# Performance work log

Hardware: AMD Instinct MI355X
Metric: run time of the kernel (lower is better)

Reference implementation:

```python
import jax, jax.numpy as jnp
import numpy as np

E = 8        # num_experts
H = 2048     # hidden_size
I = 1408     # expert_intermediate_size
SI = 2816    # shared intermediate = I * num_shared_experts
K = 2        # top_k


def swiglu(x):
    a, b = jnp.split(x, 2, axis=-1)
    return jax.nn.silu(a) * b


def setup_inputs() -> dict:
    key = jax.random.key(0)
    ks = jax.random.split(key, 8)
    hidden_states = jax.random.normal(ks[0], (2, 2048, H), dtype=jnp.float32)
    topk_weight = jax.random.uniform(ks[1], (2, 2048, K), dtype=jnp.float32)
    topk_idx = jax.random.randint(ks[2], (2, 2048, K), 0, E)
    s = 0.02
    W1 = jax.random.normal(ks[3], (E, H, 2 * I), dtype=jnp.float32) * s   # per-expert h->2i (swiglu)
    W2 = jax.random.normal(ks[4], (E, I, H), dtype=jnp.float32) * s      # per-expert i->h
    Ws1 = jax.random.normal(ks[5], (H, 2 * SI), dtype=jnp.float32) * s   # shared h->2*si
    Ws2 = jax.random.normal(ks[6], (SI, H), dtype=jnp.float32) * s       # shared si->h
    return {"hidden_states": hidden_states, "topk_weight": topk_weight,
            "W1": W1, "W2": W2, "Ws1": Ws1, "Ws2": Ws2, "topk_idx": topk_idx}


def reference(hidden_states, topk_weight, W1, W2, Ws1, Ws2, topk_idx):
    orig_shape = hidden_states.shape
    x = hidden_states.reshape(-1, H)                       # [T, h]
    T = x.shape[0]
    # run every expert on every token (dense, faithful to masked-loop math)
    h1 = jnp.einsum('th,ehf->tef', x, W1)                  # [T, E, 2i]
    act = swiglu(h1)                                       # [T, E, i]
    expert_out = jnp.einsum('tei,eih->teh', act, W2)       # [T, E, h]
    # combine weights: comb[t,e] = sum_j topk_weight[t,j] * 1[topk_idx[t,j]==e]
    onehot = jax.nn.one_hot(topk_idx.reshape(T, K), E, dtype=x.dtype)  # [T, K, E]
    comb = jnp.einsum('tk,tke->te', topk_weight.reshape(T, K), onehot)
    y = jnp.einsum('te,teh->th', comb, expert_out)         # [T, h]
    # shared experts MLP on identity
    y = y + swiglu(x @ Ws1) @ Ws2
    return y.reshape(orig_shape)
```

## Files before the change

### kernel.cpp

```cpp
#include <hip/hip_runtime.h>
#include <cmath>

#define E_    8
#define H_    2048
#define IH    1408
#define I2    2816
#define SIH   2816
#define SI2   5632
#define KTOP  2
#define T_    4096
#define NA    (T_*KTOP)
#define MAXR  (NA + E_*256)

typedef __attribute__((ext_vector_type(4)))  short  short4v;
typedef __attribute__((ext_vector_type(8)))  __bf16 bf16x8;
typedef __attribute__((ext_vector_type(4)))  float  f32x4;
typedef unsigned short bf16r;

__device__ __forceinline__ bf16r f2b(float f) {
    unsigned int u = __float_as_uint(f);
    return (bf16r)((u + 0x7FFFu + ((u >> 16) & 1u)) >> 16);
}
__device__ __forceinline__ float b2f(bf16r s) {
    return __uint_as_float(((unsigned int)s) << 16);
}

__device__ __forceinline__ void gld16(const bf16r* g, void* l) {
    __builtin_amdgcn_global_load_lds((const __attribute__((address_space(1))) void*)g,
                                     (__attribute__((address_space(3))) void*)l, 16, 0, 0);
}
__device__ __forceinline__ void barrier_raw() { asm volatile("s_barrier" ::: "memory"); }
template<int N> __device__ __forceinline__ void vmwait() {
    asm volatile("s_waitcnt vmcnt(%0)" :: "i"(N) : "memory");
}

__global__ void route_k(const int* __restrict__ idx, const float* __restrict__ tw,
                        int* __restrict__ route) {
    __shared__ int cnt[E_], cur[E_], offs[E_ + 1];
    int t = threadIdx.x;
    if (t < E_) { cnt[t] = 0; cur[t] = 0; }
    float* wrow = (float*)(route + 64 + MAXR);
    for (int i = t; i < MAXR; i += 256) { route[64 + i] = -1; wrow[i] = 0.f; }
    __syncthreads();
    for (int a = t; a < NA; a += 256) atomicAdd(&cnt[idx[a]], 1);
    __syncthreads();
    if (t == 0) {
        int run = 0;
        for (int e = 0; e < E_; e++) { offs[e] = run; run += ((cnt[e] + 255) >> 8) << 8; }
        offs[E_] = run;
    }
    __syncthreads();
    for (int a = t; a < NA; a += 256) {
        int e = idx[a];
        int p = atomicAdd(&cur[e], 1);
        int r = offs[e] + p;
        route[64 + r] = a / KTOP;
        wrow[r] = tw[a];
    }
    if (t <= E_) route[32 + t] = offs[t];
}

__global__ void cvt_k(const float* __restrict__ in, bf16r* __restrict__ out, int n4) {
    int i = blockIdx.x * 256 + threadIdx.x;
    if (i < n4) {
        float4 v = ((const float4*)in)[i];
        short4v o;
        o[0] = (short)f2b(v.x); o[1] = (short)f2b(v.y);
        o[2] = (short)f2b(v.z); o[3] = (short)f2b(v.w);
        ((short4v*)out)[i] = o;
    }
}

__global__ void tconv_k(const float* __restrict__ in, bf16r* __restrict__ out,
                        int R, int C, long ims, long oms) {
    __shared__ bf16r tile[64][65];
    const float* inp = in + blockIdx.z * ims;
    bf16r* outp = out + blockIdx.z * oms;
    int c0 = blockIdx.x * 64, r0 = blockIdx.y * 64;
    int tx = threadIdx.x, ty = threadIdx.y;
    #pragma unroll
    for (int j = 0; j < 16; j++) {
        int r = ty * 16 + j;
        tile[r][tx] = f2b(inp[(long)(r0 + r) * C + c0 + tx]);
    }
    __syncthreads();
    #pragma unroll
    for (int j = 0; j < 16; j++) {
        int c = ty * 16 + j;
        outp[(long)(c0 + c) * R + r0 + tx] = tile[tx][c];
    }
}


#define PH_READ_A(MH) { _Pragma("unroll") for (int i4 = 0; i4 < 4; i4++) \
                        _Pragma("unroll") for (int kk = 0; kk < 2; kk++) \
                            af[i4][kk] = rdA(cur, (MH), i4, kk); }
#define PH_READ_B(NH) { _Pragma("unroll") for (int j2 = 0; j2 < NJ2; j2++) \
                        _Pragma("unroll") for (int kk = 0; kk < 2; kk++) \
                            bf[(NH)][j2][kk] = rdB(cur, (NH), j2, kk); }
#define PH_MMA(MH, NH) { __builtin_amdgcn_s_setprio(1); \
    _Pragma("unroll") for (int i4 = 0; i4 < 4; i4++) \
    _Pragma("unroll") for (int j2 = 0; j2 < NJ2; j2++) \
    _Pragma("unroll") for (int kk = 0; kk < 2; kk++) \
        acc[(MH)][(NH)][i4][j2] = __builtin_amdgcn_mfma_f32_16x16x32_bf16( \
            af[i4][kk], bf[(NH)][j2][kk], acc[(MH)][(NH)][i4][j2], 0, 0, 0); \
    __builtin_amdgcn_s_setprio(0); }

template<int BNv, int KD, bool GATHER, bool ROUTED, bool PAIRED, int EPI>
__global__ __launch_bounds__(512, 2)
void g8_k(const bf16r* __restrict__ A,
          const bf16r* __restrict__ Bt, long bstride, int F,
          void* __restrict__ Cv, int ldc,
          const int* __restrict__ off, const int* __restrict__ perm,
          const float* __restrict__ wrow, int gM)
{
    constexpr int NJ2 = BNv / 128;
    constexpr int LB  = NJ2;
    constexpr int BHE = BNv * 32;
    constexpr int NT  = KD / 64;
    constexpr int W0  = (BNv == 256) ? 10 : 8;
    constexpr int W2  = (BNv == 256) ? 12 : 9;
    static_assert(!PAIRED || NJ2 == 2, "paired swiglu needs BN=256");
    static_assert(NT >= 3 && (NT & 1) == 0, "even K-tile count");

    extern __shared__ __align__(16) char smem[];
    bf16r* lA = (bf16r*)smem;
    bf16r* lB = (bf16r*)(smem + 65536);

    int nwg = gridDim.x, orig = blockIdx.x;
    int q8 = nwg >> 3, r8 = nwg & 7, xc = orig & 7, o8 = orig >> 3;
    int wgid = (xc < r8 ? xc * (q8 + 1) : r8 * (q8 + 1) + (xc - r8) * q8) + o8;
    int mt = wgid % gM, nt = wgid / gM;
    const int r0 = mt * 256;
    int e = 0;
    if (ROUTED) {
        if (r0 >= off[E_]) return;
        while (e + 1 < E_ && off[e + 1] <= r0) e++;
    }
    const bf16r* Bte = ROUTED ? Bt + (long)e * bstride : Bt;

    const int tid  = threadIdx.x;
    const int lane = tid & 63;
    const int wave = tid >> 6;
    const int wm = wave >> 2, wn = wave & 3;
    const int ml = lane & 15, kg = lane >> 4;
    const int srw  = lane >> 3;
    const int ksrc = ((lane & 7) ^ srw) * 8;

    const bf16r* pA[2][2];
    #pragma unroll
    for (int h = 0; h < 2; h++)
        #pragma unroll
        for (int l = 0; l < 2; l++) {
            int gr = r0 + h * 128 + (wave + 8 * l) * 8 + srw;
            long rw = gr;
            if (GATHER) { int tk = perm[gr]; rw = (tk < 0) ? 0 : tk; }
            pA[h][l] = A + rw * (long)KD + ksrc;
        }
    const bf16r* pB[2][LB];
    #pragma unroll
    for (int nh = 0; nh < 2; nh++)
        #pragma unroll
        for (int l = 0; l < LB; l++) {
            int lr = (wave + 8 * l) * 8 + srw;
            long gr;
            if (PAIRED) {
                int wn_ = lr >> 5, j2_ = (lr >> 4) & 1, ml_ = lr & 15;
                gr = (long)(nt * 128 + nh * 64 + wn_ * 16 + ml_) + (j2_ ? (long)F : 0L);
            } else if (NJ2 == 2) gr = (long)(nt * 256 + nh * 128 + lr);
            else                 gr = (long)(nt * 128 + nh * 64  + lr);
            pB[nh][l] = Bte + gr * (long)KD + ksrc;
        }

    auto stgA = [&](int b, int h, int kp) {
        char* d = smem + ((b * 2 + h) << 14) + (wave << 10);
        gld16(pA[h][0] + kp, d);
        gld16(pA[h][1] + kp, d + 8192);
    };
    auto stgB = [&](int b, int nh, int kp) {
        char* d = smem + 65536 + (b * 2 + nh) * (BHE * 2) + (wave << 10);
        gld16(pB[nh][0] + kp, d);
        if constexpr (LB == 2) gld16(pB[nh][1] + kp, d + 8192);
    };
    auto rdA = [&](int b, int mh, int i4, int kk) -> bf16x8 {
        int row = wm * 64 + i4 * 16 + ml;
        int u = kk * 4 + kg;
        int ee = ((b * 2 + mh) << 13) + row * 64 + ((u ^ (row & 7)) << 3);
        return *(const bf16x8*)&lA[ee];
    };
    auto rdB = [&](int b, int nh, int j2, int kk) -> bf16x8 {
        int rb = (NJ2 == 2) ? (wn * 32 + j2 * 16 + ml) : (wn * 16 + ml);
        int u = kk * 4 + kg;
        int ee = (b * 2 + nh) * BHE + rb * 64 + ((u ^ (rb & 7)) << 3);
        return *(const bf16x8*)&lB[ee];
    };

    f32x4 acc[2][2][4][NJ2];
    #pragma unroll
    for (int a0 = 0; a0 < 2; a0++)
        #pragma unroll
        for (int b0 = 0; b0 < 2; b0++)
            #pragma unroll
            for (int i = 0; i < 4; i++)
                #pragma unroll
                for (int j = 0; j < NJ2; j++)
                    acc[a0][b0][i][j] = f32x4{0.f, 0.f, 0.f, 0.f};

    bf16x8 af[4][2], bf[2][NJ2][2];

    vmwait<0>();
    stgA(0, 0, 0); stgB(0, 0, 0); stgB(0, 1, 0);
    stgA(0, 1, 0);
    stgA(1, 0, 64); stgB(1, 0, 64); stgB(1, 1, 64);

    #pragma unroll 2
    for (int t = 0; t < NT; t++) {
        const int cur = t & 1, nxt = cur ^ 1;
        const int k1 = ((t + 1 < NT) ? (t + 1) : (NT - 1)) * 64;
        const int k2 = ((t + 2 < NT) ? (t + 2) : (NT - 1)) * 64;
        stgA(nxt, 1, k1);
        vmwait<W0>(); barrier_raw();
        PH_READ_A(0); PH_READ_B(0);
        PH_MMA(0, 0);
        barrier_raw();
        stgA(cur, 0, k2);
        barrier_raw();
        PH_READ_B(1);
        PH_MMA(0, 1);
        barrier_raw();
        stgB(cur, 0, k2);
        vmwait<W2>(); barrier_raw();
        PH_READ_A(1);
        PH_MMA(1, 0);
        barrier_raw();
        stgB(cur, 1, k2);
        barrier_raw();
        PH_MMA(1, 1);
        barrier_raw();
    }

    const long colbase = (long)nt * (PAIRED ? 128 : BNv);
    #pragma unroll
    for (int mh = 0; mh < 2; mh++)
        #pragma unroll
        for (int i4 = 0; i4 < 4; i4++)
            #pragma unroll
            for (int rr = 0; rr < 4; rr++) {
                long row = (long)r0 + mh * 128 + wm * 64 + i4 * 16 + kg * 4 + rr;
                if constexpr (PAIRED) {
                    bf16r* ap = (bf16r*)Cv + row * (long)ldc + colbase;
                    #pragma unroll
                    for (int nh = 0; nh < 2; nh++) {
                        float g = acc[mh][nh][i4][0][rr];
                        float u = acc[mh][nh][i4][1][rr];
                        float s = g / (1.0f + __expf(-g));
                        ap[nh * 64 + wn * 16 + ml] = f2b(s * u);
                    }
                } else if constexpr (EPI == 1) {
                    float* cp = (float*)Cv + row * (long)ldc + colbase;
                    #pragma unroll
                    for (int nh = 0; nh < 2; nh++)
                        #pragma unroll
                        for (int j2 = 0; j2 < NJ2; j2++)
                            cp[nh * (BNv / 2) + wn * (BNv / 8) + j2 * 16 + ml] =
                                acc[mh][nh][i4][j2][rr];
                } else {
                    int tok = perm[row];
                    if (tok >= 0) {
                        float w = wrow[row];
                        float* cp = (float*)Cv + (long)tok * ldc + colbase;
                        #pragma unroll
                        for (int nh = 0; nh < 2; nh++)
                            #pragma unroll
                            for (int j2 = 0; j2 < NJ2; j2++)
                                atomicAdd(&cp[nh * (BNv / 2) + wn * (BNv / 8) + j2 * 16 + ml],
                                          w * acc[mh][nh][i4][j2][rr]);
                    }
                }
            }
}

#undef PH_READ_A
#undef PH_READ_B
#undef PH_MMA

extern "C" void kernel_launch(void* const* d_in, const int* in_sizes, int n_in,
                              void* d_out, int out_size, void* d_ws, size_t ws_size,
                              hipStream_t stream)
{
    const float* x   = (const float*)d_in[0];
    const float* tw  = (const float*)d_in[1];
    const float* W1  = (const float*)d_in[2];
    const float* W2  = (const float*)d_in[3];
    const float* Ws1 = (const float*)d_in[4];
    const float* Ws2 = (const float*)d_in[5];
    const int*   tix = (const int*)d_in[6];
    float* out = (float*)d_out;

    char* ws    = (char*)d_ws;
    int*  route = (int*)ws;
    const int*   off  = route + 32;
    const int*   perm = route + 64;
    const float* wrow = (const float*)(route + 64 + MAXR);

    bf16r* xb   = (bf16r*)(ws + (1u << 20));
    bf16r* W1t  = xb   + (size_t)T_ * H_;
    bf16r* W2t  = W1t  + (size_t)E_ * I2 * H_;
    bf16r* Ws1t = W2t  + (size_t)E_ * H_ * IH;
    bf16r* Ws2t = Ws1t + (size_t)SI2 * H_;
    bf16r* actS = Ws2t + (size_t)H_ * SIH;
    bf16r* actR = actS + (size_t)T_ * SIH;

    static bool attr_done = false;
    if (!attr_done) {
        hipFuncSetAttribute(reinterpret_cast<const void*>(&g8_k<256,2048,false,false,true,0>),
                            hipFuncAttributeMaxDynamicSharedMemorySize, 131072);
        hipFuncSetAttribute(reinterpret_cast<const void*>(&g8_k<256,2048,true,true,true,0>),
                            hipFuncAttributeMaxDynamicSharedMemorySize, 131072);
        hipFuncSetAttribute(reinterpret_cast<const void*>(&g8_k<128,2816,false,false,false,1>),
                            hipFuncAttributeMaxDynamicSharedMemorySize, 98304);
        hipFuncSetAttribute(reinterpret_cast<const void*>(&g8_k<256,1408,false,true,false,2>),
                            hipFuncAttributeMaxDynamicSharedMemorySize, 131072);
        attr_done = true;
    }

    route_k<<<1, 256, 0, stream>>>(tix, tw, route);

    cvt_k<<<(T_ * H_ / 4 + 255) / 256, 256, 0, stream>>>(x, xb, T_ * H_ / 4);
    tconv_k<<<dim3(SI2 / 64, H_ / 64, 1), dim3(64, 4), 0, stream>>>(Ws1, Ws1t, H_, SI2, 0, 0);
    tconv_k<<<dim3(H_ / 64, SIH / 64, 1), dim3(64, 4), 0, stream>>>(Ws2, Ws2t, SIH, H_, 0, 0);
    tconv_k<<<dim3(I2 / 64, H_ / 64, E_), dim3(64, 4), 0, stream>>>(W1, W1t, H_, I2,
                                                                    (long)H_ * I2, (long)I2 * H_);
    tconv_k<<<dim3(H_ / 64, IH / 64, E_), dim3(64, 4), 0, stream>>>(W2, W2t, IH, H_,
                                                                    (long)IH * H_, (long)H_ * IH);

    g8_k<256,2048,false,false,true,0><<<dim3((SIH/128)*(T_/256)), dim3(512), 131072, stream>>>(
        xb, Ws1t, 0, SIH, actS, SIH, nullptr, nullptr, nullptr, T_/256);
    g8_k<128,2816,false,false,false,1><<<dim3((H_/128)*(T_/256)), dim3(512), 98304, stream>>>(
        actS, Ws2t, 0, 0, out, H_, nullptr, nullptr, nullptr, T_/256);
    g8_k<256,2048,true,true,true,0><<<dim3((IH/128)*(MAXR/256)), dim3(512), 131072, stream>>>(
        xb, W1t, (long)I2 * H_, IH, actR, IH, off, perm, nullptr, MAXR/256);
    g8_k<256,1408,false,true,false,2><<<dim3((H_/256)*(MAXR/256)), dim3(512), 131072, stream>>>(
        actR, W2t, (long)H_ * IH, 0, out, H_, off, perm, wrow, MAXR/256);
}
```

Baseline: 813.1 us.

## Restructure GEMM pipeline prefetch ordering and replace scatter atomics with bf16 staging plus combine

The GEMM main loop is reordered so LDS fragment reads for each phase are issued before the next global-to-LDS stage, with double-buffered A fragments and a uniform vmcnt wait, aiming to overlap LDS reads with MFMA and memory traffic better. The routed down-projection epilogue no longer does fp32 atomicAdd scatters into the output. It writes weighted results in bf16 to a per-row staging buffer that reuses the W1t region, and a new comb_k kernel gathers the two rows per token and adds them to the output. This removes atomic contention but adds an extra kernel plus bf16 rounding of the expert outputs before the sum.

```diff
diff --git a/kernel.cpp b/kernel.cpp
--- a/kernel.cpp
+++ b/kernel.cpp
@@ -40,6 +40,7 @@
     int t = threadIdx.x;
     if (t < E_) { cnt[t] = 0; cur[t] = 0; }
     float* wrow = (float*)(route + 64 + MAXR);
+    int* pos = route + 64 + 2 * MAXR;
     for (int i = t; i < MAXR; i += 256) { route[64 + i] = -1; wrow[i] = 0.f; }
     __syncthreads();
     for (int a = t; a < NA; a += 256) atomicAdd(&cnt[idx[a]], 1);
@@ -56,6 +57,7 @@
         int r = offs[e] + p;
         route[64 + r] = a / KTOP;
         wrow[r] = tw[a];
+        pos[a] = r;
     }
     if (t <= E_) route[32 + t] = offs[t];
 }
@@ -91,19 +93,35 @@
     }
 }
 
+__global__ void comb_k(float* __restrict__ out, const bf16r* __restrict__ outR,
+                       const int* __restrict__ pos) {
+    int i = blockIdx.x * 256 + threadIdx.x;
+    int t  = i >> 9;
+    int c4 = i & 511;
+    int p0 = pos[2 * t], p1 = pos[2 * t + 1];
+    float4 o = ((float4*)out)[i];
+    short4v r0 = ((const short4v*)(outR + (long)p0 * H_))[c4];
+    short4v r1 = ((const short4v*)(outR + (long)p1 * H_))[c4];
+    o.x += b2f((bf16r)r0[0]) + b2f((bf16r)r1[0]);
+    o.y += b2f((bf16r)r0[1]) + b2f((bf16r)r1[1]);
+    o.z += b2f((bf16r)r0[2]) + b2f((bf16r)r1[2]);
+    o.w += b2f((bf16r)r0[3]) + b2f((bf16r)r1[3]);
+    ((float4*)out)[i] = o;
+}
+
 
 #define PH_READ_A(MH) { _Pragma("unroll") for (int i4 = 0; i4 < 4; i4++) \
                         _Pragma("unroll") for (int kk = 0; kk < 2; kk++) \
-                            af[i4][kk] = rdA(cur, (MH), i4, kk); }
+                            af[(MH)][i4][kk] = rdA(cur, (MH), i4, kk); }
 #define PH_READ_B(NH) { _Pragma("unroll") for (int j2 = 0; j2 < NJ2; j2++) \
                         _Pragma("unroll") for (int kk = 0; kk < 2; kk++) \
-                            bf[(NH)][j2][kk] = rdB(cur, (NH), j2, kk); }
+                            bfr[(NH)][j2][kk] = rdB(cur, (NH), j2, kk); }
 #define PH_MMA(MH, NH) { __builtin_amdgcn_s_setprio(1); \
     _Pragma("unroll") for (int i4 = 0; i4 < 4; i4++) \
     _Pragma("unroll") for (int j2 = 0; j2 < NJ2; j2++) \
     _Pragma("unroll") for (int kk = 0; kk < 2; kk++) \
         acc[(MH)][(NH)][i4][j2] = __builtin_amdgcn_mfma_f32_16x16x32_bf16( \
-            af[i4][kk], bf[(NH)][j2][kk], acc[(MH)][(NH)][i4][j2], 0, 0, 0); \
+            af[(MH)][i4][kk], bfr[(NH)][j2][kk], acc[(MH)][(NH)][i4][j2], 0, 0, 0); \
     __builtin_amdgcn_s_setprio(0); }
 
 template<int BNv, int KD, bool GATHER, bool ROUTED, bool PAIRED, int EPI>
@@ -118,10 +136,9 @@
     constexpr int LB  = NJ2;
     constexpr int BHE = BNv * 32;
     constexpr int NT  = KD / 64;
-    constexpr int W0  = (BNv == 256) ? 10 : 8;
-    constexpr int W2  = (BNv == 256) ? 12 : 9;
+    constexpr int VW  = 4 + 2 * LB;
     static_assert(!PAIRED || NJ2 == 2, "paired swiglu needs BN=256");
-    static_assert(NT >= 3 && (NT & 1) == 0, "even K-tile count");
+    static_assert(NT >= 4 && (NT & 1) == 0, "even K-tile count >= 4");
 
     extern __shared__ __align__(16) char smem[];
     bf16r* lA = (bf16r*)smem;
@@ -206,38 +223,42 @@
                 for (int j = 0; j < NJ2; j++)
                     acc[a0][b0][i][j] = f32x4{0.f, 0.f, 0.f, 0.f};
 
-    bf16x8 af[4][2], bf[2][NJ2][2];
+    bf16x8 af[2][4][2], bfr[2][NJ2][2];
 
     vmwait<0>();
-    stgA(0, 0, 0); stgB(0, 0, 0); stgB(0, 1, 0);
-    stgA(0, 1, 0);
-    stgA(1, 0, 64); stgB(1, 0, 64); stgB(1, 1, 64);
+    stgA(0, 0, 0); stgB(0, 0, 0); stgB(0, 1, 0); stgA(0, 1, 0);
+    stgA(1, 0, 64); stgB(1, 0, 64);
+    vmwait<LB + 2>(); barrier_raw();
 
     #pragma unroll 2
     for (int t = 0; t < NT; t++) {
         const int cur = t & 1, nxt = cur ^ 1;
         const int k1 = ((t + 1 < NT) ? (t + 1) : (NT - 1)) * 64;
         const int k2 = ((t + 2 < NT) ? (t + 2) : (NT - 1)) * 64;
+        PH_READ_A(0); PH_READ_B(0);
+        stgB(nxt, 1, k1);
+        vmwait<VW>();
+        barrier_raw();
+        PH_MMA(0, 0);
+        barrier_raw();
+        PH_READ_B(1);
         stgA(nxt, 1, k1);
-        vmwait<W0>(); barrier_raw();
-        PH_READ_A(0); PH_READ_B(0);
-        PH_MMA(0, 0);
-        barrier_raw();
+        vmwait<VW>();
+        barrier_raw();
+        PH_MMA(0, 1);
+        barrier_raw();
+        PH_READ_A(1);
         stgA(cur, 0, k2);
         barrier_raw();
-        PH_READ_B(1);
-        PH_MMA(0, 1);
+        PH_MMA(1, 0);
         barrier_raw();
         stgB(cur, 0, k2);
-        vmwait<W2>(); barrier_raw();
-        PH_READ_A(1);
-        PH_MMA(1, 0);
-        barrier_raw();
-        stgB(cur, 1, k2);
+        vmwait<VW>();
         barrier_raw();
         PH_MMA(1, 1);
         barrier_raw();
     }
+    vmwait<0>();
 
     const long colbase = (long)nt * (PAIRED ? 128 : BNv);
     #pragma unroll
@@ -268,13 +289,13 @@
                     int tok = perm[row];
                     if (tok >= 0) {
                         float w = wrow[row];
-                        float* cp = (float*)Cv + (long)tok * ldc + colbase;
+                        bf16r* cp = (bf16r*)Cv + row * (long)ldc + colbase;
                         #pragma unroll
                         for (int nh = 0; nh < 2; nh++)
                             #pragma unroll
                             for (int j2 = 0; j2 < NJ2; j2++)
-                                atomicAdd(&cp[nh * (BNv / 2) + wn * (BNv / 8) + j2 * 16 + ml],
-                                          w * acc[mh][nh][i4][j2][rr]);
+                                cp[nh * (BNv / 2) + wn * (BNv / 8) + j2 * 16 + ml] =
+                                    f2b(w * acc[mh][nh][i4][j2][rr]);
                     }
                 }
             }
@@ -302,6 +323,7 @@
     const int*   off  = route + 32;
     const int*   perm = route + 64;
     const float* wrow = (const float*)(route + 64 + MAXR);
+    const int*   pos  = route + 64 + 2 * MAXR;
 
     bf16r* xb   = (bf16r*)(ws + (1u << 20));
     bf16r* W1t  = xb   + (size_t)T_ * H_;
@@ -310,6 +332,7 @@
     bf16r* Ws2t = Ws1t + (size_t)SI2 * H_;
     bf16r* actS = Ws2t + (size_t)H_ * SIH;
     bf16r* actR = actS + (size_t)T_ * SIH;
+    bf16r* outR = W1t;
 
     static bool attr_done = false;
     if (!attr_done) {
@@ -341,5 +364,6 @@
     g8_k<256,2048,true,true,true,0><<<dim3((IH/128)*(MAXR/256)), dim3(512), 131072, stream>>>(
         xb, W1t, (long)I2 * H_, IH, actR, IH, off, perm, nullptr, MAXR/256);
     g8_k<256,1408,false,true,false,2><<<dim3((H_/256)*(MAXR/256)), dim3(512), 131072, stream>>>(
-        actR, W2t, (long)H_ * IH, 0, out, H_, off, perm, wrow, MAXR/256);
-}
+        actR, W2t, (long)H_ * IH, 0, outR, H_, off, perm, wrow, MAXR/256);
+    comb_k<<<T_ * H_ / 4 / 256, 256, 0, stream>>>(out, outR, pos);
+}
```

Measured after the change: 816.7 us. No clear change (+0.4%).
